# Kernel optimization log

Hardware: AMD Instinct MI355X
Metric: run time of the kernel (lower is better)

## Reference

```python
import math
import jax, jax.numpy as jnp
import numpy as np

EPS = 1e-6

def rmsnorm(x, g):
    # RMSNorm: x / rms(x) * g
    return x * jax.lax.rsqrt(jnp.mean(x * x, axis=-1, keepdims=True) + EPS) * g

def setup_inputs() -> dict:
    key = jax.random.key(0)
    ks = jax.random.split(key, 10)
    B, S, D, H = 1, 4096, 1024, 16
    dh = D // H
    s = 0.02  # init scale for weights
    x = jax.random.normal(ks[0], (B, S, D), dtype=jnp.float32)
    # causal mask: masked_fill(mask == 0, -inf) => lower-triangular ones
    mask = jnp.tril(jnp.ones((S, S), dtype=jnp.int32))
    WQ = jax.random.normal(ks[1], (H, D, dh), dtype=jnp.float32) * s
    WK = jax.random.normal(ks[2], (H, D, dh), dtype=jnp.float32) * s
    WV = jax.random.normal(ks[3], (H, D, dh), dtype=jnp.float32) * s
    WO = jax.random.normal(ks[4], (D, D), dtype=jnp.float32) * s
    W1 = jax.random.normal(ks[5], (D, 4 * D), dtype=jnp.float32) * s
    B1 = jnp.zeros((4 * D,), dtype=jnp.float32)
    W2 = jax.random.normal(ks[6], (4 * D, D), dtype=jnp.float32) * s
    B2 = jnp.zeros((D,), dtype=jnp.float32)
    g1 = jnp.ones((D,), dtype=jnp.float32)
    g2 = jnp.ones((D,), dtype=jnp.float32)
    return {"x": x, "mask": mask, "g1": g1, "WQ": WQ, "WK": WK, "WV": WV,
            "WO": WO, "g2": g2, "W1": W1, "B1": B1, "W2": W2, "B2": B2}

def reference(x, mask, g1, WQ, WK, WV, WO, g2, W1, B1, W2, B2):
    dh = WQ.shape[-1]
    # --- attention sub-block (pre-norm) ---
    h = rmsnorm(x, g1)                                   # [B,S,D]
    Q = jnp.einsum('bsd,hde->bhse', h, WQ)               # [B,H,S,dh]
    K = jnp.einsum('bsd,hde->bhse', h, WK)
    V = jnp.einsum('bsd,hde->bhse', h, WV)
    # rope() in the source is identity
    scores = jnp.einsum('bhse,bhte->bhst', Q, K) / math.sqrt(dh)  # [B,H,S,S]
    scores = jnp.where(mask == 0, -jnp.inf, scores)
    attn = jax.nn.softmax(scores, axis=-1)
    o = jnp.einsum('bhst,bhte->bhse', attn, V)           # [B,H,S,dh]
    Bn, H, S, e = o.shape
    o = o.transpose(0, 2, 1, 3).reshape(Bn, S, H * e)    # concat heads on last dim
    x = x + o @ WO
    # --- MLP sub-block (pre-norm) ---
    h2 = rmsnorm(x, g2)
    m = jax.nn.relu(h2 @ W1 + B1) @ W2 + B2
    return x + m
```

## Files before the change

### kernel.cpp

```cpp
#include <hip/hip_runtime.h>
#include <hip/hip_bf16.h>

typedef __attribute__((ext_vector_type(8))) short bf16x8;
typedef __attribute__((ext_vector_type(4))) float f32x4;
typedef __attribute__((ext_vector_type(4))) short s16x4;

#define GLOBAL_AS(p) ((const __attribute__((address_space(1))) void*)(p))
#define LDS_AS(p)    ((__attribute__((address_space(3))) void*)(p))

__device__ __forceinline__ short f2bf(float f) {
  return __builtin_bit_cast(short, __float2bfloat16(f));
}
__device__ __forceinline__ float bf2f(short s) {
  return __bfloat162float(__builtin_bit_cast(__hip_bfloat16, s));
}

__global__ __launch_bounds__(256) void pack_qkv_kernel(
    const float* __restrict__ WQ, const float* __restrict__ WK,
    const float* __restrict__ WV, short* __restrict__ out) {
  __shared__ short Ls[64][66];
  const int tid = threadIdx.x;
  const int l = tid & 63, q4 = tid >> 6;
  const int hh = blockIdx.y & 15, proj = blockIdx.y >> 4;
  const float* W = (proj == 0) ? WQ : ((proj == 1) ? WK : WV);
  const float scl = (proj == 0) ? 0.125f : 1.f;
  const int d0 = blockIdx.x * 64;
#pragma unroll
  for (int rep = 0; rep < 16; ++rep) {
    int dd = q4 * 16 + rep;
    Ls[dd][l] = f2bf(W[(size_t)hh * 65536 + (size_t)(d0 + dd) * 64 + l] * scl);
  }
  __syncthreads();
#pragma unroll
  for (int rep = 0; rep < 16; ++rep) {
    int ee = q4 * 16 + rep;
    out[(size_t)(proj * 1024 + hh * 64 + ee) * 1024 + d0 + l] = Ls[l][ee];
  }
}

__global__ __launch_bounds__(256) void transpose_bf16_kernel(
    const float* __restrict__ in, short* __restrict__ out, int R, int C) {
  __shared__ short Ls[64][66];
  const int tid = threadIdx.x;
  const int l = tid & 63, q4 = tid >> 6;
  const int c0 = blockIdx.x * 64, r0 = blockIdx.y * 64;
#pragma unroll
  for (int rep = 0; rep < 16; ++rep) {
    int rr = q4 * 16 + rep;
    Ls[rr][l] = f2bf(in[(size_t)(r0 + rr) * C + c0 + l]);
  }
  __syncthreads();
#pragma unroll
  for (int rep = 0; rep < 16; ++rep) {
    int cc = q4 * 16 + rep;
    out[(size_t)(c0 + cc) * R + r0 + l] = Ls[l][cc];
  }
}

__global__ __launch_bounds__(256) void transpose_v_kernel(
    const short* __restrict__ qkv, short* __restrict__ vt, int S) {
  __shared__ short Ls[64][66];
  const int tid = threadIdx.x;
  const int l = tid & 63, q4 = tid >> 6;
  const int s0 = blockIdx.x * 64, e0 = blockIdx.y * 64;
#pragma unroll
  for (int rep = 0; rep < 16; ++rep) {
    int rr = q4 * 16 + rep;
    Ls[rr][l] = qkv[(size_t)(s0 + rr) * 3072 + 2048 + e0 + l];
  }
  __syncthreads();
#pragma unroll
  for (int rep = 0; rep < 16; ++rep) {
    int ee = q4 * 16 + rep;
    vt[(size_t)(e0 + ee) * S + s0 + l] = Ls[l][ee];
  }
}

__global__ __launch_bounds__(256) void rmsnorm_kernel(
    const float* __restrict__ x, const float* __restrict__ g,
    short* __restrict__ out, int D) {
  const int row = blockIdx.x;
  const int tid = threadIdx.x;
  const float4 xv = *(const float4*)&x[(size_t)row * D + tid * 4];
  float ss = xv.x * xv.x + xv.y * xv.y + xv.z * xv.z + xv.w * xv.w;
#pragma unroll
  for (int off = 32; off; off >>= 1) ss += __shfl_xor(ss, off);
  __shared__ float red[4];
  if ((tid & 63) == 0) red[tid >> 6] = ss;
  __syncthreads();
  float tot = red[0] + red[1] + red[2] + red[3];
  float scale = rsqrtf(tot / (float)D + 1e-6f);
  const float4 gv = *(const float4*)&g[tid * 4];
  s16x4 o;
  o[0] = f2bf(xv.x * scale * gv.x);
  o[1] = f2bf(xv.y * scale * gv.y);
  o[2] = f2bf(xv.z * scale * gv.z);
  o[3] = f2bf(xv.w * scale * gv.w);
  *(s16x4*)&out[(size_t)row * D + tid * 4] = o;
}

template <int EPI>
__global__ __launch_bounds__(256) void gemm_bt_kernel(
    const short* __restrict__ A, const short* __restrict__ BT,
    int M, int N, int K,
    short* __restrict__ outB, float* __restrict__ outF,
    const float* __restrict__ bias, const float* __restrict__ addend) {
  __shared__ short As[128 * 32];
  __shared__ short Bs[128 * 32];
  const int tid = threadIdx.x;
  const int lane = tid & 63;
  const int wid = tid >> 6;
  const int lrow = lane & 15;
  const int kk = lane >> 4;
  const int row0 = blockIdx.y * 128;
  const int col0 = blockIdx.x * 128;
  const int wm = wid >> 1, wn = wid & 1;

  f32x4 acc[4][4] = {};

  for (int k0 = 0; k0 < K; k0 += 32) {
    __syncthreads();
#pragma unroll
    for (int it = 0; it < 2; ++it) {
      int c = it * 256 + tid;
      int r = c >> 2, c8 = (c & 3) * 8;
      const short* ga = A + (size_t)(row0 + r) * K + k0 + c8;
      const short* gb = BT + (size_t)(col0 + r) * K + k0 + c8;
      short* la = &As[(size_t)(it * 256 + wid * 64) * 8];
      short* lb = &Bs[(size_t)(it * 256 + wid * 64) * 8];
      __builtin_amdgcn_global_load_lds(GLOBAL_AS(ga), LDS_AS(la), 16, 0, 0);
      __builtin_amdgcn_global_load_lds(GLOBAL_AS(gb), LDS_AS(lb), 16, 0, 0);
    }
    __syncthreads();

    bf16x8 a[4], b[4];
#pragma unroll
    for (int i = 0; i < 4; ++i)
      a[i] = *(const bf16x8*)&As[(wm * 64 + i * 16 + lrow) * 32 + kk * 8];
#pragma unroll
    for (int i = 0; i < 4; ++i)
      b[i] = *(const bf16x8*)&Bs[(wn * 64 + i * 16 + lrow) * 32 + kk * 8];
#pragma unroll
    for (int i = 0; i < 4; ++i)
#pragma unroll
      for (int j = 0; j < 4; ++j)
        acc[i][j] = __builtin_amdgcn_mfma_f32_16x16x32_bf16(a[i], b[j], acc[i][j], 0, 0, 0);
  }

#pragma unroll
  for (int i = 0; i < 4; ++i) {
    int row = row0 + wm * 64 + i * 16 + kk * 4;
#pragma unroll
    for (int j = 0; j < 4; ++j) {
      int col = col0 + wn * 64 + j * 16 + lrow;
#pragma unroll
      for (int r = 0; r < 4; ++r) {
        float v = acc[i][j][r];
        size_t o = (size_t)(row + r) * N + col;
        if (EPI == 0) {
          outB[o] = f2bf(v);
        } else if (EPI == 1) {
          outF[o] = v + addend[o];
        } else if (EPI == 2) {
          v += bias[col];
          outB[o] = f2bf(v > 0.f ? v : 0.f);
        } else {
          outF[o] = v + bias[col] + addend[o];
        }
      }
    }
  }
}

#define READ_A(buf, mh)                                                      \
  _Pragma("unroll") for (int m4 = 0; m4 < 4; ++m4) {                         \
    int row_ = wm * 128 + ((mh)*4 + m4) * 16 + lrow;                         \
    _Pragma("unroll") for (int k_ = 0; k_ < 2; ++k_) {                       \
      int sl_ = (k_ * 4 + kk) ^ (row_ & 7);                                  \
      aA[m4][k_] = *(const bf16x8*)&lds[buf][0][row_ * 64 + sl_ * 8];        \
    }                                                                        \
  }
#define READ_B2(buf, pr)                                                     \
  _Pragma("unroll") for (int nn = 0; nn < 2; ++nn) {                         \
    int n_ = (pr)*2 + nn;                                                    \
    int row_ = wn * 64 + n_ * 16 + lrow;                                     \
    _Pragma("unroll") for (int k_ = 0; k_ < 2; ++k_) {                       \
      int sl_ = (k_ * 4 + kk) ^ (row_ & 7);                                  \
      bB[n_][k_] = *(const bf16x8*)&lds[buf][1][row_ * 64 + sl_ * 8];        \
    }                                                                        \
  }
#define MFMA16(mh, nh)                                                       \
  _Pragma("unroll") for (int m4 = 0; m4 < 4; ++m4)                           \
  _Pragma("unroll") for (int n2 = 0; n2 < 2; ++n2)                           \
  _Pragma("unroll") for (int k_ = 0; k_ < 2; ++k_)                           \
    acc[(mh)*4 + m4][(nh)*2 + n2] = __builtin_amdgcn_mfma_f32_16x16x32_bf16( \
        aA[m4][k_], bB[(nh)*2 + n2][k_], acc[(mh)*4 + m4][(nh)*2 + n2], 0, 0, 0);
#define STAGE_HALF(buf, mat, half, kt)                                       \
  {                                                                          \
    const short* g_ = ((mat) ? Bb : Ab) + (size_t)((half)*128) * K + (kt)*64;\
    short* l_ = &lds[buf][mat][(half)*8192];                                 \
    _Pragma("unroll") for (int it_ = 0; it_ < 2; ++it_) {                    \
      int ci_ = it_ * 512 + tid;                                             \
      int r_ = ci_ >> 3, sl_ = (ci_ & 7) ^ (r_ & 7);                         \
      __builtin_amdgcn_global_load_lds(GLOBAL_AS(g_ + (size_t)r_ * K + sl_ * 8), \
                                       LDS_AS(l_ + ci_ * 8), 16, 0, 0);      \
    }                                                                        \
  }
#define PH_SYNC1()                                                           \
  __builtin_amdgcn_s_barrier();                                              \
  asm volatile("s_waitcnt lgkmcnt(0)" ::: "memory");                         \
  __builtin_amdgcn_sched_barrier(0);                                         \
  __builtin_amdgcn_s_setprio(1)
#define PH_SYNC2()                                                           \
  __builtin_amdgcn_s_setprio(0);                                             \
  __builtin_amdgcn_s_barrier()
#define PH_SYNC2_VM(n)                                                       \
  __builtin_amdgcn_s_setprio(0);                                             \
  asm volatile("s_waitcnt vmcnt(" #n ")" ::: "memory");                      \
  __builtin_amdgcn_s_barrier()

template <int EPI>
__global__ __launch_bounds__(512, 2) void gemm256_kernel(
    const short* __restrict__ A, const short* __restrict__ BT,
    int N, int K, int kslice, size_t pstride,
    short* __restrict__ outB, const float* __restrict__ bias) {
  __shared__ short lds[2][2][16384];
  const int tid = threadIdx.x;
  const int lane = tid & 63, wid = tid >> 6;
  const int lrow = lane & 15, kk = lane >> 4;
  const int wm = wid >> 2, wn = wid & 3;
  const int row0 = blockIdx.y * 256, col0 = blockIdx.x * 256;
  const int kbase = blockIdx.z * kslice;
  const int NT = kslice >> 6;

  const short* Ab = A + (size_t)row0 * K + kbase;
  const short* Bb = BT + (size_t)col0 * K + kbase;

  f32x4 acc[8][4] = {};
  bf16x8 aA[4][2], bB[4][2];

  STAGE_HALF(0, 1, 0, 0); STAGE_HALF(0, 0, 0, 0);
  STAGE_HALF(0, 1, 1, 0); STAGE_HALF(0, 0, 1, 0);
  STAGE_HALF(1, 1, 0, 1); STAGE_HALF(1, 0, 0, 1); STAGE_HALF(1, 0, 1, 1);
  asm volatile("s_waitcnt vmcnt(6)" ::: "memory");
  __builtin_amdgcn_s_barrier();

  const int iters = NT >> 1;
  for (int i = 0; i < iters; ++i) {
    const int t1 = 2 * i + 1;
    int kt2 = 2 * i + 2; if (kt2 >= NT) kt2 -= NT;
    int kt3 = 2 * i + 3; if (kt3 >= NT) kt3 -= NT;
    READ_A(0, 0); READ_B2(0, 0); STAGE_HALF(1, 1, 1, t1);
    PH_SYNC1(); MFMA16(0, 0); PH_SYNC2();
    READ_B2(0, 1);
    PH_SYNC1(); MFMA16(0, 1); PH_SYNC2();
    READ_A(0, 1); STAGE_HALF(0, 1, 0, kt2);
    PH_SYNC1(); MFMA16(1, 0); PH_SYNC2();
    STAGE_HALF(0, 0, 0, kt2);
    PH_SYNC1(); MFMA16(1, 1); PH_SYNC2_VM(4);
    READ_A(1, 0); READ_B2(1, 0); STAGE_HALF(0, 1, 1, kt2);
    PH_SYNC1(); MFMA16(0, 0); PH_SYNC2();
    READ_B2(1, 1); STAGE_HALF(0, 0, 1, kt2);
    PH_SYNC1(); MFMA16(0, 1); PH_SYNC2();
    READ_A(1, 1); STAGE_HALF(1, 1, 0, kt3);
    PH_SYNC1(); MFMA16(1, 0); PH_SYNC2();
    STAGE_HALF(1, 0, 0, kt3); STAGE_HALF(1, 0, 1, kt3);
    PH_SYNC1(); MFMA16(1, 1); PH_SYNC2_VM(6);
  }

  short* ob = outB + (size_t)blockIdx.z * pstride;
#pragma unroll
  for (int m = 0; m < 8; ++m) {
    int row = row0 + wm * 128 + m * 16 + kk * 4;
#pragma unroll
    for (int n = 0; n < 4; ++n) {
      int col = col0 + wn * 64 + n * 16 + lrow;
#pragma unroll
      for (int r = 0; r < 4; ++r) {
        float v = acc[m][n][r];
        size_t o = (size_t)(row + r) * N + col;
        if (EPI == 0) {
          ob[o] = f2bf(v);
        } else {
          v += bias[col];
          ob[o] = f2bf(v > 0.f ? v : 0.f);
        }
      }
    }
  }
}

__global__ __launch_bounds__(256) void reduce4_kernel(
    const short* __restrict__ part, const float* __restrict__ bias,
    const float* __restrict__ addend, float* __restrict__ out) {
  const size_t MN = (size_t)4096 * 1024;
  size_t i8 = ((size_t)blockIdx.x * 256 + threadIdx.x) * 8;
  bf16x8 p0 = *(const bf16x8*)&part[i8];
  bf16x8 p1 = *(const bf16x8*)&part[MN + i8];
  bf16x8 p2 = *(const bf16x8*)&part[2 * MN + i8];
  bf16x8 p3 = *(const bf16x8*)&part[3 * MN + i8];
  int col = (int)(i8 & 1023);
#pragma unroll
  for (int j = 0; j < 8; ++j) {
    float v = (bf2f(p0[j]) + bf2f(p1[j])) + (bf2f(p2[j]) + bf2f(p3[j]));
    out[i8 + j] = v + bias[col + j] + addend[i8 + j];
  }
}

__device__ const unsigned char QT_SLOT[48] = {
    31, 31, 30, 15, 30, 29, 29, 28, 14, 28, 27, 27, 26, 13, 26, 25,
    25, 24, 12, 24, 23, 23, 22, 11, 22, 21, 21, 20, 10, 20, 19, 19,
    18,  9, 18, 17, 17, 16,  8, 16,  7,  6,  5,  4,  3,  2,  1,  0};
__device__ const unsigned char SP_SLOT[48] = {
    0, 1, 0, 0, 1, 0, 1, 0, 0, 1, 0, 1, 0, 0, 1, 0,
    1, 0, 0, 1, 0, 1, 0, 0, 1, 0, 1, 0, 0, 1, 0, 1,
    0, 0, 1, 0, 1, 0, 0, 1, 0, 0, 0, 0, 0, 0, 0, 0};

__global__ __launch_bounds__(512, 4) void attn_kernel(
    const short* __restrict__ QKV, const short* __restrict__ VT,
    float* __restrict__ opart, float* __restrict__ lpart) {
  const int S = 4096;
  __shared__ short Ks[2][128 * 64];
  __shared__ short Vs[2][64 * 128];
  __shared__ short Ps[8][16 * 64];

  const int tid = threadIdx.x;
  const int lane = tid & 63;
  const int w = tid >> 6;
  const int lrow = lane & 15;
  const int kk = lane >> 4;
  const int bid = blockIdx.x;
  const int h = bid & 15;
  const int slot = bid >> 4;
  const int qtile = QT_SLOT[slot];
  const int sp = SP_SLOT[slot];
  const int T = qtile + 1;
  const bool split = (qtile >= 16);
  const int half = (T + 1) >> 1;
  const int t0 = (split && sp) ? half : 0;
  const int t1 = (split && !sp) ? half : T;
  const int q0 = qtile * 128;
  const int qw = q0 + w * 16;

  auto stage = [&](int buf, int t) {
    const int kv0 = t * 128;
#pragma unroll
    for (int it = 0; it < 2; ++it) {
      int ci = it * 512 + tid;
      int krow = ci >> 3;
      int ksl = (ci & 7) ^ (krow & 7);
      int vrow = ci >> 4;
      int vsl = (ci & 15) ^ (vrow & 15);
      const short* gk = QKV + (size_t)(kv0 + krow) * 3072 + 1024 + h * 64 + ksl * 8;
      const short* gv = VT + (size_t)(h * 64 + vrow) * S + kv0 + vsl * 8;
      __builtin_amdgcn_global_load_lds(GLOBAL_AS(gk),
                                       LDS_AS(&Ks[buf][(it * 512 + w * 64) * 8]), 16, 0, 0);
      __builtin_amdgcn_global_load_lds(GLOBAL_AS(gv),
                                       LDS_AS(&Vs[buf][(it * 512 + w * 64) * 8]), 16, 0, 0);
    }
  };

  bf16x8 qf[2];
#pragma unroll
  for (int half2 = 0; half2 < 2; ++half2)
    qf[half2] = *(const bf16x8*)&QKV[(size_t)(qw + lrow) * 3072 +
                                     h * 64 + half2 * 32 + kk * 8];

  float rs_acc[4] = {};
  f32x4 o_acc[4] = {};

  stage(0, t0);
  __syncthreads();
  int cur = 0;

  for (int t = t0; t < t1; ++t) {
    if (t + 1 < t1) stage(cur ^ 1, t + 1);

#pragma unroll
    for (int h2 = 0; h2 < 2; ++h2) {
      const int kvc = t * 128 + h2 * 64;
      if (kvc > qw + 15) continue;

      bf16x8 kf[4][2];
#pragma unroll
      for (int c = 0; c < 4; ++c)
#pragma unroll
        for (int half2 = 0; half2 < 2; ++half2) {
          int krow = h2 * 64 + c * 16 + lrow;
          kf[c][half2] = *(const bf16x8*)&Ks[cur][krow * 64 + (((half2 * 4 + kk) ^ (lrow & 7)) * 8)];
        }
      f32x4 sc[4];
      __builtin_amdgcn_s_setprio(1);
#pragma unroll
      for (int c = 0; c < 4; ++c) {
        f32x4 z = {};
        z = __builtin_amdgcn_mfma_f32_16x16x32_bf16(qf[0], kf[c][0], z, 0, 0, 0);
        z = __builtin_amdgcn_mfma_f32_16x16x32_bf16(qf[1], kf[c][1], z, 0, 0, 0);
        sc[c] = z;
      }
      __builtin_amdgcn_s_setprio(0);

      if (kvc + 63 <= qw) {
#pragma unroll
        for (int r = 0; r < 4; ++r) {
          const int qrow = kk * 4 + r;
          float ps[4];
#pragma unroll
          for (int c = 0; c < 4; ++c) {
            float p = __expf(sc[c][r]);
            ps[c] = p;
            int col = c * 16 + lrow;
            Ps[w][qrow * 64 + (((col >> 3) ^ (qrow & 7)) * 8) + (col & 7)] = f2bf(p);
          }
          rs_acc[r] += (ps[0] + ps[1]) + (ps[2] + ps[3]);
        }
      } else {
#pragma unroll
        for (int r = 0; r < 4; ++r) {
          const int qrow = kk * 4 + r;
          const int q = qw + qrow;
          float ps[4];
#pragma unroll
          for (int c = 0; c < 4; ++c) {
            float p = __expf(sc[c][r]);
            if (kvc + c * 16 + lrow > q) p = 0.f;
            ps[c] = p;
            int col = c * 16 + lrow;
            Ps[w][qrow * 64 + (((col >> 3) ^ (qrow & 7)) * 8) + (col & 7)] = f2bf(p);
          }
          rs_acc[r] += (ps[0] + ps[1]) + (ps[2] + ps[3]);
        }
      }

#pragma unroll
      for (int ks = 0; ks < 2; ++ks) {
        bf16x8 pf2, vf[4];
        {
          int qrow = lrow;
          pf2 = *(const bf16x8*)&Ps[w][qrow * 64 + (((ks * 4 + kk) ^ (qrow & 7)) * 8)];
        }
#pragma unroll
        for (int g = 0; g < 4; ++g) {
          int erow = g * 16 + lrow;
          vf[g] = *(const bf16x8*)&Vs[cur][erow * 128 + (((h2 * 8 + ks * 4 + kk) ^ (lrow & 15)) * 8)];
        }
        __builtin_amdgcn_s_setprio(1);
#pragma unroll
        for (int g = 0; g < 4; ++g)
          o_acc[g] = __builtin_amdgcn_mfma_f32_16x16x32_bf16(pf2, vf[g], o_acc[g], 0, 0, 0);
        __builtin_amdgcn_s_setprio(0);
      }
    }

    __syncthreads();
    cur ^= 1;
  }

  const int pidx = (h * 32 + qtile) * 2 + sp;
  float* op = opart + (size_t)pidx * 8192;
  float* lp = lpart + pidx * 128;
#pragma unroll
  for (int r = 0; r < 4; ++r) {
    float l = rs_acc[r];
    l += __shfl_xor(l, 1);
    l += __shfl_xor(l, 2);
    l += __shfl_xor(l, 4);
    l += __shfl_xor(l, 8);
    if (lrow == 0) lp[w * 16 + kk * 4 + r] = l;
  }
#pragma unroll
  for (int g = 0; g < 4; ++g)
#pragma unroll
    for (int r = 0; r < 4; ++r)
      op[(w * 16 + kk * 4 + r) * 64 + g * 16 + lrow] = o_acc[g][r];
}

__global__ __launch_bounds__(256) void attn_combine_kernel(
    const float* __restrict__ opart, const float* __restrict__ lpart,
    short* __restrict__ O) {
  size_t e8 = ((size_t)blockIdx.x * 256 + threadIdx.x) * 8;
  const int srow = (int)(e8 >> 10);
  const int col = (int)(e8 & 1023);
  const int h = col >> 6, d = col & 63;
  const int qtile = srow >> 7, qr = srow & 127;
  const int pb = (h * 32 + qtile) * 2;
  const float* o0 = opart + (size_t)pb * 8192 + qr * 64 + d;
  float l = lpart[pb * 128 + qr];
  float4 a0 = *(const float4*)o0;
  float4 a1 = *(const float4*)(o0 + 4);
  if (qtile >= 16) {
    const float* o1 = opart + (size_t)(pb + 1) * 8192 + qr * 64 + d;
    float4 b0 = *(const float4*)o1;
    float4 b1 = *(const float4*)(o1 + 4);
    a0.x += b0.x; a0.y += b0.y; a0.z += b0.z; a0.w += b0.w;
    a1.x += b1.x; a1.y += b1.y; a1.z += b1.z; a1.w += b1.w;
    l += lpart[(pb + 1) * 128 + qr];
  }
  float inv = 1.f / l;
  bf16x8 o;
  o[0] = f2bf(a0.x * inv); o[1] = f2bf(a0.y * inv);
  o[2] = f2bf(a0.z * inv); o[3] = f2bf(a0.w * inv);
  o[4] = f2bf(a1.x * inv); o[5] = f2bf(a1.y * inv);
  o[6] = f2bf(a1.z * inv); o[7] = f2bf(a1.w * inv);
  *(bf16x8*)&O[e8] = o;
}

extern "C" void kernel_launch(void* const* d_in, const int* in_sizes, int n_in,
                              void* d_out, int out_size, void* d_ws, size_t ws_size,
                              hipStream_t stream) {
  const float* x  = (const float*)d_in[0];
  const float* g1 = (const float*)d_in[2];
  const float* WQ = (const float*)d_in[3];
  const float* WK = (const float*)d_in[4];
  const float* WV = (const float*)d_in[5];
  const float* WO = (const float*)d_in[6];
  const float* g2 = (const float*)d_in[7];
  const float* W1 = (const float*)d_in[8];
  const float* B1 = (const float*)d_in[9];
  const float* W2 = (const float*)d_in[10];
  const float* B2 = (const float*)d_in[11];
  float* out = (float*)d_out;

  const int S = 4096, D = 1024, H = 16;

  char* ws = (char*)d_ws;
  size_t off = 0;
  auto alloc = [&](size_t bytes) -> void* {
    void* p = ws + off;
    off += (bytes + 255) & ~(size_t)255;
    return p;
  };
  short* h1     = (short*)alloc((size_t)S * D * 2);
  short* wqkv_t = (short*)alloc((size_t)3072 * 1024 * 2);
  short* qkv    = (short*)alloc((size_t)S * 3072 * 2);
  short* vt     = (short*)alloc((size_t)1024 * S * 2);
  short* attn_o = (short*)alloc((size_t)S * D * 2);
  short* wo_t   = (short*)alloc((size_t)1024 * 1024 * 2);
  float* x2     = (float*)alloc((size_t)S * D * 4);
  short* h2     = (short*)alloc((size_t)S * D * 2);
  short* w1_t   = (short*)alloc((size_t)4096 * 1024 * 2);
  short* m1     = (short*)alloc((size_t)S * 4096 * 2);
  short* w2_t   = (short*)alloc((size_t)1024 * 4096 * 2);
  short* partW2 = qkv;
  float* opart  = (float*)m1;
  float* lpart  = (float*)h1;

  pack_qkv_kernel<<<dim3(D / 64, 48), 256, 0, stream>>>(WQ, WK, WV, wqkv_t);
  transpose_bf16_kernel<<<dim3(1024 / 64, 1024 / 64), 256, 0, stream>>>(WO, wo_t, 1024, 1024);
  transpose_bf16_kernel<<<dim3(4096 / 64, 1024 / 64), 256, 0, stream>>>(W1, w1_t, 1024, 4096);
  transpose_bf16_kernel<<<dim3(1024 / 64, 4096 / 64), 256, 0, stream>>>(W2, w2_t, 4096, 1024);

  rmsnorm_kernel<<<S, 256, 0, stream>>>(x, g1, h1, D);
  gemm256_kernel<0><<<dim3(3072 / 256, S / 256, 1), 512, 0, stream>>>(
      h1, wqkv_t, 3072, 1024, 1024, 0, qkv, nullptr);
  transpose_v_kernel<<<dim3(S / 64, 1024 / 64), 256, 0, stream>>>(qkv, vt, S);
  attn_kernel<<<dim3(768), 512, 0, stream>>>(qkv, vt, opart, lpart);
  attn_combine_kernel<<<dim3((S * 1024 / 8) / 256), 256, 0, stream>>>(opart, lpart, attn_o);
  gemm_bt_kernel<1><<<dim3(1024 / 128, S / 128), 256, 0, stream>>>(
      attn_o, wo_t, S, 1024, 1024, nullptr, x2, nullptr, x);

  rmsnorm_kernel<<<S, 256, 0, stream>>>(x2, g2, h2, D);
  gemm256_kernel<2><<<dim3(4096 / 256, 4096 / 256, 1), 512, 0, stream>>>(
      h2, w1_t, 4096, 1024, 1024, 0, m1, B1);
  gemm256_kernel<0><<<dim3(1024 / 256, 4096 / 256, 4), 512, 0, stream>>>(
      m1, w2_t, 1024, 4096, 1024, (size_t)4096 * 1024, partW2, nullptr);
  reduce4_kernel<<<2048, 256, 0, stream>>>(partW2, B2, x2, out);
}
```

Baseline: 249.5 us.

## Transpose QK score MFMA and normalize unsplit attention tiles in-kernel

The QK^T MFMA now runs with operands swapped, so each lane holds four consecutive keys for one query row. P is written to LDS as packed 4-element stores and the row sum needs only two cross-lane shuffles. Unsplit query tiles (first half of the sequence) normalize and write bf16 output directly, so the combine kernel only handles the split second half. This cuts fp32 partial traffic and scalar LDS stores, at the cost of extra per-row shuffles in the epilogue.

```diff
diff --git a/kernel.cpp b/kernel.cpp
--- a/kernel.cpp
+++ b/kernel.cpp
@@ -318,7 +318,8 @@
 
 __global__ __launch_bounds__(512, 4) void attn_kernel(
     const short* __restrict__ QKV, const short* __restrict__ VT,
-    float* __restrict__ opart, float* __restrict__ lpart) {
+    float* __restrict__ opart, float* __restrict__ lpart,
+    short* __restrict__ O) {
   const int S = 4096;
   __shared__ short Ks[2][128 * 64];
   __shared__ short Vs[2][64 * 128];
@@ -341,6 +342,7 @@
   const int t1 = (split && !sp) ? half : T;
   const int q0 = qtile * 128;
   const int qw = q0 + w * 16;
+  const int myq = qw + lrow;
 
   auto stage = [&](int buf, int t) {
     const int kv0 = t * 128;
@@ -366,7 +368,7 @@
     qf[half2] = *(const bf16x8*)&QKV[(size_t)(qw + lrow) * 3072 +
                                      h * 64 + half2 * 32 + kk * 8];
 
-  float rs_acc[4] = {};
+  float rs_acc = 0.f;
   f32x4 o_acc[4] = {};
 
   stage(0, t0);
@@ -394,41 +396,39 @@
 #pragma unroll
       for (int c = 0; c < 4; ++c) {
         f32x4 z = {};
-        z = __builtin_amdgcn_mfma_f32_16x16x32_bf16(qf[0], kf[c][0], z, 0, 0, 0);
-        z = __builtin_amdgcn_mfma_f32_16x16x32_bf16(qf[1], kf[c][1], z, 0, 0, 0);
+        z = __builtin_amdgcn_mfma_f32_16x16x32_bf16(kf[c][0], qf[0], z, 0, 0, 0);
+        z = __builtin_amdgcn_mfma_f32_16x16x32_bf16(kf[c][1], qf[1], z, 0, 0, 0);
         sc[c] = z;
       }
       __builtin_amdgcn_s_setprio(0);
 
       if (kvc + 63 <= qw) {
 #pragma unroll
-        for (int r = 0; r < 4; ++r) {
-          const int qrow = kk * 4 + r;
-          float ps[4];
-#pragma unroll
-          for (int c = 0; c < 4; ++c) {
+        for (int c = 0; c < 4; ++c) {
+          float p0 = __expf(sc[c][0]), p1 = __expf(sc[c][1]);
+          float p2 = __expf(sc[c][2]), p3 = __expf(sc[c][3]);
+          rs_acc += (p0 + p1) + (p2 + p3);
+          s16x4 pk;
+          pk[0] = f2bf(p0); pk[1] = f2bf(p1); pk[2] = f2bf(p2); pk[3] = f2bf(p3);
+          int slot8 = c * 2 + (kk >> 1);
+          *(s16x4*)&Ps[w][lrow * 64 + ((slot8 ^ (lrow & 7)) * 8) + (kk & 1) * 4] = pk;
+        }
+      } else {
+#pragma unroll
+        for (int c = 0; c < 4; ++c) {
+          const int keyb = kvc + c * 16 + kk * 4;
+          float pv[4];
+#pragma unroll
+          for (int r = 0; r < 4; ++r) {
             float p = __expf(sc[c][r]);
-            ps[c] = p;
-            int col = c * 16 + lrow;
-            Ps[w][qrow * 64 + (((col >> 3) ^ (qrow & 7)) * 8) + (col & 7)] = f2bf(p);
+            if (keyb + r > myq) p = 0.f;
+            pv[r] = p;
           }
-          rs_acc[r] += (ps[0] + ps[1]) + (ps[2] + ps[3]);
-        }
-      } else {
-#pragma unroll
-        for (int r = 0; r < 4; ++r) {
-          const int qrow = kk * 4 + r;
-          const int q = qw + qrow;
-          float ps[4];
-#pragma unroll
-          for (int c = 0; c < 4; ++c) {
-            float p = __expf(sc[c][r]);
-            if (kvc + c * 16 + lrow > q) p = 0.f;
-            ps[c] = p;
-            int col = c * 16 + lrow;
-            Ps[w][qrow * 64 + (((col >> 3) ^ (qrow & 7)) * 8) + (col & 7)] = f2bf(p);
-          }
-          rs_acc[r] += (ps[0] + ps[1]) + (ps[2] + ps[3]);
+          rs_acc += (pv[0] + pv[1]) + (pv[2] + pv[3]);
+          s16x4 pk;
+          pk[0] = f2bf(pv[0]); pk[1] = f2bf(pv[1]); pk[2] = f2bf(pv[2]); pk[3] = f2bf(pv[3]);
+          int slot8 = c * 2 + (kk >> 1);
+          *(s16x4*)&Ps[w][lrow * 64 + ((slot8 ^ (lrow & 7)) * 8) + (kk & 1) * 4] = pk;
         }
       }
 
@@ -456,46 +456,53 @@
     cur ^= 1;
   }
 
-  const int pidx = (h * 32 + qtile) * 2 + sp;
-  float* op = opart + (size_t)pidx * 8192;
-  float* lp = lpart + pidx * 128;
-#pragma unroll
-  for (int r = 0; r < 4; ++r) {
-    float l = rs_acc[r];
-    l += __shfl_xor(l, 1);
-    l += __shfl_xor(l, 2);
-    l += __shfl_xor(l, 4);
-    l += __shfl_xor(l, 8);
-    if (lrow == 0) lp[w * 16 + kk * 4 + r] = l;
-  }
-#pragma unroll
-  for (int g = 0; g < 4; ++g)
-#pragma unroll
-    for (int r = 0; r < 4; ++r)
-      op[(w * 16 + kk * 4 + r) * 64 + g * 16 + lrow] = o_acc[g][r];
+  float l = rs_acc;
+  l += __shfl_xor(l, 16);
+  l += __shfl_xor(l, 32);
+
+  if (!split) {
+    float inv_[4];
+#pragma unroll
+    for (int r = 0; r < 4; ++r) inv_[r] = 1.f / __shfl(l, kk * 4 + r);
+#pragma unroll
+    for (int g = 0; g < 4; ++g)
+#pragma unroll
+      for (int r = 0; r < 4; ++r) {
+        int s_idx = qw + kk * 4 + r;
+        O[(size_t)s_idx * 1024 + h * 64 + g * 16 + lrow] =
+            f2bf(o_acc[g][r] * inv_[r]);
+      }
+  } else {
+    const int pidx = (h * 32 + qtile) * 2 + sp;
+    float* op = opart + (size_t)pidx * 8192;
+    float* lp = lpart + pidx * 128;
+    if (lane < 16) lp[w * 16 + lrow] = l;
+#pragma unroll
+    for (int g = 0; g < 4; ++g)
+#pragma unroll
+      for (int r = 0; r < 4; ++r)
+        op[(w * 16 + kk * 4 + r) * 64 + g * 16 + lrow] = o_acc[g][r];
+  }
 }
 
 __global__ __launch_bounds__(256) void attn_combine_kernel(
     const float* __restrict__ opart, const float* __restrict__ lpart,
     short* __restrict__ O) {
-  size_t e8 = ((size_t)blockIdx.x * 256 + threadIdx.x) * 8;
+  size_t e8 = ((size_t)blockIdx.x * 256 + threadIdx.x) * 8 + (size_t)2048 * 1024;
   const int srow = (int)(e8 >> 10);
   const int col = (int)(e8 & 1023);
   const int h = col >> 6, d = col & 63;
   const int qtile = srow >> 7, qr = srow & 127;
   const int pb = (h * 32 + qtile) * 2;
   const float* o0 = opart + (size_t)pb * 8192 + qr * 64 + d;
-  float l = lpart[pb * 128 + qr];
+  const float* o1 = opart + (size_t)(pb + 1) * 8192 + qr * 64 + d;
+  float l = lpart[pb * 128 + qr] + lpart[(pb + 1) * 128 + qr];
   float4 a0 = *(const float4*)o0;
   float4 a1 = *(const float4*)(o0 + 4);
-  if (qtile >= 16) {
-    const float* o1 = opart + (size_t)(pb + 1) * 8192 + qr * 64 + d;
-    float4 b0 = *(const float4*)o1;
-    float4 b1 = *(const float4*)(o1 + 4);
-    a0.x += b0.x; a0.y += b0.y; a0.z += b0.z; a0.w += b0.w;
-    a1.x += b1.x; a1.y += b1.y; a1.z += b1.z; a1.w += b1.w;
-    l += lpart[(pb + 1) * 128 + qr];
-  }
+  float4 b0 = *(const float4*)o1;
+  float4 b1 = *(const float4*)(o1 + 4);
+  a0.x += b0.x; a0.y += b0.y; a0.z += b0.z; a0.w += b0.w;
+  a1.x += b1.x; a1.y += b1.y; a1.z += b1.z; a1.w += b1.w;
   float inv = 1.f / l;
   bf16x8 o;
   o[0] = f2bf(a0.x * inv); o[1] = f2bf(a0.y * inv);
@@ -554,8 +561,8 @@
   gemm256_kernel<0><<<dim3(3072 / 256, S / 256, 1), 512, 0, stream>>>(
       h1, wqkv_t, 3072, 1024, 1024, 0, qkv, nullptr);
   transpose_v_kernel<<<dim3(S / 64, 1024 / 64), 256, 0, stream>>>(qkv, vt, S);
-  attn_kernel<<<dim3(768), 512, 0, stream>>>(qkv, vt, opart, lpart);
-  attn_combine_kernel<<<dim3((S * 1024 / 8) / 256), 256, 0, stream>>>(opart, lpart, attn_o);
+  attn_kernel<<<dim3(768), 512, 0, stream>>>(qkv, vt, opart, lpart, attn_o);
+  attn_combine_kernel<<<dim3((2048 * 1024 / 8) / 256), 256, 0, stream>>>(opart, lpart, attn_o);
   gemm_bt_kernel<1><<<dim3(1024 / 128, S / 128), 256, 0, stream>>>(
       attn_o, wo_t, S, 1024, 1024, nullptr, x2, nullptr, x);
 
```

New measurement: 244.3 us. -2.1%, faster.
